# Kernel optimization log

Measured on AMD Instinct MI355X. Metric: run time of the kernel, lower is better.

The kernel has to match this reference:

```python
import jax, jax.numpy as jnp
import numpy as np

ALPHA = 0.2  # LeakyReLU negative slope


def setup_inputs() -> dict:
    key = jax.random.key(0)
    k1, k2, k3, k4 = jax.random.split(key, 4)
    B, N, IN_F, OUT_F = 8, 2048, 128, 64
    inputs = jax.random.normal(k1, (B, N, IN_F), dtype=jnp.float32)
    nodes_embedding = jax.random.normal(k2, (B, N, OUT_F), dtype=jnp.float32)
    # xavier-uniform-like init (gain 1.414)
    limW = 1.414 * np.sqrt(6.0 / (IN_F + OUT_F))
    W = jax.random.uniform(k3, (IN_F, OUT_F), dtype=jnp.float32, minval=-limW, maxval=limW)
    lima = 1.414 * np.sqrt(6.0 / (4 * OUT_F + 1))
    a = jax.random.uniform(k4, (4 * OUT_F, 1), dtype=jnp.float32, minval=-lima, maxval=lima)
    return {"inputs": inputs, "nodes_embedding": nodes_embedding, "W": W, "a": a}


def reference(inputs, nodes_embedding, W, a):
    # x_w: [B,N,F]
    x_w = jnp.matmul(inputs, W)
    # h: [B,N,2F]
    h = jnp.concatenate([nodes_embedding, x_w], axis=2)
    twoF = h.shape[-1]
    # Separable form of concat-based attention: a_input[b,i,j] = [h_i, h_j],
    # so a_input @ a = (h_i . a1) + (h_j . a2). Avoids the O(B*N^2*4F) tensor.
    a1 = a[:twoF, 0]  # [2F]
    a2 = a[twoF:, 0]  # [2F]
    s1 = jnp.einsum('bnf,f->bn', h, a1)  # [B,N]
    s2 = jnp.einsum('bnf,f->bn', h, a2)  # [B,N]
    e = jax.nn.leaky_relu(s1[:, :, None] + s2[:, None, :], negative_slope=ALPHA)  # [B,N,N]
    attention = jax.nn.softmax(e, axis=2)  # softmax over j
    # dropout: eval mode (training=False) -> identity
    h_prime = jnp.matmul(attention, x_w)  # [B,N,F]
    return (jax.nn.relu(h_prime), attention)
```

## Files before the change

### kernel.cpp

```cpp
#include <hip/hip_runtime.h>

#define ALPHA 0.2f
#define B_    8
#define N_    2048
#define INF_  128
#define OUTF_ 64
#define LOG2E 1.4426950408889634f

typedef __attribute__((ext_vector_type(8))) short short8;
typedef __attribute__((ext_vector_type(4))) float f32x4;

__device__ __forceinline__ unsigned short f2bf(float f) {
    unsigned int x = __float_as_uint(f);
    return (unsigned short)((x + 0x7fffu + ((x >> 16) & 1u)) >> 16);
}

__device__ __forceinline__ unsigned int cvtpk_bf16(float lo, float hi) {
    unsigned int r;
    asm("v_cvt_pk_bf16_f32 %0, %1, %2" : "=v"(r) : "v"(lo), "v"(hi));
    return r;
}

__global__ __launch_bounds__(256) void prep_kernel(
    const float* __restrict__ inp,
    const float* __restrict__ nodes,
    const float* __restrict__ Wm,
    const float* __restrict__ av,
    unsigned short* __restrict__ xwT,
    float* __restrict__ s1_out,
    float* __restrict__ s2_out)
{
    __shared__ float w_lds[INF_ * OUTF_];
    __shared__ float in_lds[16 * INF_];
    __shared__ __align__(16) unsigned short t_lds[64 * 16];
    const int tid  = threadIdx.x;
    const int wave = tid >> 6, lane = tid & 63;
    const int r0   = blockIdx.x * 16;

    {
        const float4* Wv = (const float4*)Wm;
        float4* wd = (float4*)w_lds;
        #pragma unroll
        for (int q = 0; q < 8; q++) wd[tid + q * 256] = Wv[tid + q * 256];
        const float4* Iv = (const float4*)(inp + (size_t)r0 * INF_);
        float4* id4 = (float4*)in_lds;
        id4[tid]       = Iv[tid];
        id4[tid + 256] = Iv[tid + 256];
    }
    __syncthreads();

    float acc[4] = {0.f, 0.f, 0.f, 0.f};
    const float* inw = &in_lds[(wave * 4) * INF_];
    #pragma unroll 4
    for (int k = 0; k < INF_; k++) {
        float wv = w_lds[k * OUTF_ + lane];
        acc[0] += inw[k]            * wv;
        acc[1] += inw[INF_ + k]     * wv;
        acc[2] += inw[2 * INF_ + k] * wv;
        acc[3] += inw[3 * INF_ + k] * wv;
    }

    const float a1n = av[lane];
    const float a1x = av[64 + lane];
    const float a2n = av[128 + lane];
    const float a2x = av[192 + lane];

    #pragma unroll
    for (int rr = 0; rr < 4; rr++) {
        const int row = r0 + wave * 4 + rr;
        float nf = nodes[(size_t)row * OUTF_ + lane];
        float p1 = nf * a1n + acc[rr] * a1x;
        float p2 = nf * a2n + acc[rr] * a2x;
        #pragma unroll
        for (int off = 32; off; off >>= 1) {
            p1 += __shfl_down(p1, off);
            p2 += __shfl_down(p2, off);
        }
        if (lane == 0) { s1_out[row] = p1; s2_out[row] = p2; }
        t_lds[lane * 16 + wave * 4 + rr] = f2bf(acc[rr]);
    }
    __syncthreads();

    {
        const int n  = tid >> 2, c0 = (tid & 3) * 4;
        const int b  = r0 >> 11, rb = r0 & (N_ - 1);
        *(uint2*)(xwT + ((size_t)b * OUTF_ + n) * N_ + rb + c0) =
            *(const uint2*)&t_lds[n * 16 + c0];
    }
}

__global__ __launch_bounds__(1024, 4) void attn_kernel(
    const unsigned short* __restrict__ xwT,
    const float* __restrict__ s1g,
    const float* __restrict__ s2g,
    float* __restrict__ out_h,
    float* __restrict__ out_att)
{
    __shared__ __align__(16) float smem[12288];
    __shared__ float s1_lds[64];
    __shared__ float c1_lds[64];
    __shared__ float c2_lds[64];
    __shared__ float redmax[16];

    float* s2L = smem;
    float* s2A = smem + 2048;
    f32x4* red = (f32x4*)smem;

    const int tid  = threadIdx.x;
    const int wave = tid >> 6, lane = tid & 63;
    const int b  = blockIdx.x & 7;
    const int i0 = (blockIdx.x >> 3) << 6;

    {
        float2 v = *(const float2*)(s2g + b * N_ + tid * 2);
        float lm = fmaxf(v.x, v.y);
        s2L[tid * 2]     = v.x * LOG2E;
        s2L[tid * 2 + 1] = v.y * LOG2E;
        s2A[tid * 2]     = v.x * (ALPHA * LOG2E);
        s2A[tid * 2 + 1] = v.y * (ALPHA * LOG2E);
        #pragma unroll
        for (int off = 32; off; off >>= 1) lm = fmaxf(lm, __shfl_xor(lm, off));
        if (lane == 0) redmax[wave] = lm;
    }
    if (tid < 64) s1_lds[tid] = s1g[b * N_ + i0 + tid];
    __syncthreads();

    float s2max = redmax[0];
    #pragma unroll
    for (int w = 1; w < 16; w++) s2max = fmaxf(s2max, redmax[w]);

    {
        const int row = tid >> 4, jo = tid & 15;
        const float s1v = s1_lds[row];
        const float vm  = s1v + s2max;
        const float mL  = (vm > 0.f ? vm : ALPHA * vm) * LOG2E;
        const float d1  = s1v * LOG2E - mL;
        const float d2  = s1v * (ALPHA * LOG2E) - mL;
        float l = 0.f;
        for (int j = jo * 4; j < N_; j += 64) {
            float4 xl = *(const float4*)&s2L[j];
            float4 xa = *(const float4*)&s2A[j];
            l += __builtin_amdgcn_exp2f(fmaxf(d1 + xl.x, d2 + xa.x));
            l += __builtin_amdgcn_exp2f(fmaxf(d1 + xl.y, d2 + xa.y));
            l += __builtin_amdgcn_exp2f(fmaxf(d1 + xl.z, d2 + xa.z));
            l += __builtin_amdgcn_exp2f(fmaxf(d1 + xl.w, d2 + xa.w));
        }
        l += __shfl_xor(l, 1);
        l += __shfl_xor(l, 2);
        l += __shfl_xor(l, 4);
        l += __shfl_xor(l, 8);
        if (jo == 0) {
            const float lg = __builtin_amdgcn_logf(l);
            c1_lds[row] = d1 - lg;
            c2_lds[row] = d2 - lg;
        }
    }
    __syncthreads();

    const int row16 = lane & 15;
    const int quad  = lane >> 4;
    const int wsub  = wave & 3;
    const int jq    = wave >> 2;
    const int irow  = wsub * 16 + row16;
    const float c1  = c1_lds[irow];
    const float c2  = c2_lds[irow];
    const int jb    = jq * 512;

    const unsigned short* bptr[4];
    #pragma unroll
    for (int g = 0; g < 4; g++)
        bptr[g] = xwT + ((size_t)b * OUTF_ + g * 16 + row16) * N_ + jb + quad * 8;

    float* attp = out_att + ((size_t)(b * N_ + i0 + irow)) * N_ + jb + quad * 8;
    const float* pL = s2L + jb + quad * 8;
    const float* pA = s2A + jb + quad * 8;

    f32x4 acc0 = {0.f,0.f,0.f,0.f}, acc1 = {0.f,0.f,0.f,0.f};
    f32x4 acc2 = {0.f,0.f,0.f,0.f}, acc3 = {0.f,0.f,0.f,0.f};

    uint4 bnext[4];
    #pragma unroll
    for (int g = 0; g < 4; g++) bnext[g] = *(const uint4*)bptr[g];

    for (int jt = 0; jt < 512; jt += 32) {
        uint4 bc0 = bnext[0], bc1 = bnext[1], bc2 = bnext[2], bc3 = bnext[3];
        const int jn = (jt + 32) & 511;
        #pragma unroll
        for (int g = 0; g < 4; g++) bnext[g] = *(const uint4*)(bptr[g] + jn);

        float4 sa = *(const float4*)(pL + jt);
        float4 sb = *(const float4*)(pL + jt + 4);
        float4 ta = *(const float4*)(pA + jt);
        float4 tb = *(const float4*)(pA + jt + 4);
        float av8[8];
        av8[0] = __builtin_amdgcn_exp2f(fmaxf(c1 + sa.x, c2 + ta.x));
        av8[1] = __builtin_amdgcn_exp2f(fmaxf(c1 + sa.y, c2 + ta.y));
        av8[2] = __builtin_amdgcn_exp2f(fmaxf(c1 + sa.z, c2 + ta.z));
        av8[3] = __builtin_amdgcn_exp2f(fmaxf(c1 + sa.w, c2 + ta.w));
        av8[4] = __builtin_amdgcn_exp2f(fmaxf(c1 + sb.x, c2 + tb.x));
        av8[5] = __builtin_amdgcn_exp2f(fmaxf(c1 + sb.y, c2 + tb.y));
        av8[6] = __builtin_amdgcn_exp2f(fmaxf(c1 + sb.z, c2 + tb.z));
        av8[7] = __builtin_amdgcn_exp2f(fmaxf(c1 + sb.w, c2 + tb.w));

        *(float4*)(attp + jt)     = make_float4(av8[0], av8[1], av8[2], av8[3]);
        *(float4*)(attp + jt + 4) = make_float4(av8[4], av8[5], av8[6], av8[7]);

        uint4 pk;
        pk.x = cvtpk_bf16(av8[0], av8[1]);
        pk.y = cvtpk_bf16(av8[2], av8[3]);
        pk.z = cvtpk_bf16(av8[4], av8[5]);
        pk.w = cvtpk_bf16(av8[6], av8[7]);
        short8 a8 = *(short8*)&pk;

        acc0 = __builtin_amdgcn_mfma_f32_16x16x32_bf16(a8, *(short8*)&bc0, acc0, 0, 0, 0);
        acc1 = __builtin_amdgcn_mfma_f32_16x16x32_bf16(a8, *(short8*)&bc1, acc1, 0, 0, 0);
        acc2 = __builtin_amdgcn_mfma_f32_16x16x32_bf16(a8, *(short8*)&bc2, acc2, 0, 0, 0);
        acc3 = __builtin_amdgcn_mfma_f32_16x16x32_bf16(a8, *(short8*)&bc3, acc3, 0, 0, 0);
    }

    __syncthreads();
    if (jq > 0) {
        f32x4* p = red + (((jq - 1) * 4 + wsub) * 64 + lane) * 4;
        p[0] = acc0; p[1] = acc1; p[2] = acc2; p[3] = acc3;
    }
    __syncthreads();
    if (jq == 0) {
        #pragma unroll
        for (int q = 0; q < 3; q++) {
            f32x4* p = red + ((q * 4 + wsub) * 64 + lane) * 4;
            acc0 += p[0]; acc1 += p[1]; acc2 += p[2]; acc3 += p[3];
        }
        const size_t hb = ((size_t)(b * N_) + i0 + wsub * 16) * OUTF_;
        #pragma unroll
        for (int r = 0; r < 4; r++) {
            const size_t ro = hb + (size_t)(quad * 4 + r) * OUTF_ + row16;
            out_h[ro]      = fmaxf(acc0[r], 0.f);
            out_h[ro + 16] = fmaxf(acc1[r], 0.f);
            out_h[ro + 32] = fmaxf(acc2[r], 0.f);
            out_h[ro + 48] = fmaxf(acc3[r], 0.f);
        }
    }
}

extern "C" void kernel_launch(void* const* d_in, const int* in_sizes, int n_in,
                              void* d_out, int out_size, void* d_ws, size_t ws_size,
                              hipStream_t stream) {
    const float* inp   = (const float*)d_in[0];
    const float* nodes = (const float*)d_in[1];
    const float* Wm    = (const float*)d_in[2];
    const float* av    = (const float*)d_in[3];

    float* out_h   = (float*)d_out;
    float* out_att = out_h + (size_t)B_ * N_ * OUTF_;

    unsigned short* xwT = (unsigned short*)d_ws;
    float* s1_ws = (float*)((char*)d_ws + (size_t)B_ * OUTF_ * N_ * sizeof(unsigned short));
    float* s2_ws = s1_ws + (size_t)B_ * N_;

    prep_kernel<<<(B_ * N_) / 16, 256, 0, stream>>>(inp, nodes, Wm, av,
                                                    xwT, s1_ws, s2_ws);
    attn_kernel<<<256, 1024, 0, stream>>>(xwT, s1_ws, s2_ws, out_h, out_att);
}
```

Before: 187.7 us.

## Write attention rows in a coalesced pass and vectorize prep matmul LDS reads

The attention-matrix store moves out of the MFMA loop into a separate pass. In that pass each wave writes whole contiguous rows with lane-strided float4 stores, replacing the old pattern of 16 rows by 4 quads per instruction. This is meant to improve write coalescing on the dominant output stream, at the cost of computing the exp values twice and adding an extra barrier. The prep kernel's small matmul also now reads input rows as float4 from LDS, with a 4-way unrolled k loop.

```diff
diff --git a/kernel.cpp b/kernel.cpp
--- a/kernel.cpp
+++ b/kernel.cpp
@@ -31,7 +31,7 @@
     float* __restrict__ s2_out)
 {
     __shared__ float w_lds[INF_ * OUTF_];
-    __shared__ float in_lds[16 * INF_];
+    __shared__ __align__(16) float in_lds[16 * INF_];
     __shared__ __align__(16) unsigned short t_lds[64 * 16];
     const int tid  = threadIdx.x;
     const int wave = tid >> 6, lane = tid & 63;
@@ -51,13 +51,20 @@
 
     float acc[4] = {0.f, 0.f, 0.f, 0.f};
     const float* inw = &in_lds[(wave * 4) * INF_];
-    #pragma unroll 4
-    for (int k = 0; k < INF_; k++) {
-        float wv = w_lds[k * OUTF_ + lane];
-        acc[0] += inw[k]            * wv;
-        acc[1] += inw[INF_ + k]     * wv;
-        acc[2] += inw[2 * INF_ + k] * wv;
-        acc[3] += inw[3 * INF_ + k] * wv;
+    #pragma unroll 2
+    for (int k = 0; k < INF_; k += 4) {
+        float4 r0v = *(const float4*)&inw[k];
+        float4 r1v = *(const float4*)&inw[INF_ + k];
+        float4 r2v = *(const float4*)&inw[2 * INF_ + k];
+        float4 r3v = *(const float4*)&inw[3 * INF_ + k];
+        float w0 = w_lds[k * OUTF_ + lane];
+        float w1 = w_lds[(k + 1) * OUTF_ + lane];
+        float w2 = w_lds[(k + 2) * OUTF_ + lane];
+        float w3 = w_lds[(k + 3) * OUTF_ + lane];
+        acc[0] += r0v.x * w0 + r0v.y * w1 + r0v.z * w2 + r0v.w * w3;
+        acc[1] += r1v.x * w0 + r1v.y * w1 + r1v.z * w2 + r1v.w * w3;
+        acc[2] += r2v.x * w0 + r2v.y * w1 + r2v.z * w2 + r2v.w * w3;
+        acc[3] += r3v.x * w0 + r3v.y * w1 + r3v.z * w2 + r3v.w * w3;
     }
 
     const float a1n = av[lane];
@@ -166,12 +173,44 @@
     const float c2  = c2_lds[irow];
     const int jb    = jq * 512;
 
+    {
+        const size_t rowbase = (size_t)(b * N_ + i0 + wsub * 16);
+        const int cl = lane * 4;
+        for (int r = 0; r < 16; r++) {
+            const float c1r = c1_lds[wsub * 16 + r];
+            const float c2r = c2_lds[wsub * 16 + r];
+            float* orow = out_att + (rowbase + r) * N_ + jb;
+            {
+                const int col = cl;
+                float4 xl = *(const float4*)&s2L[jb + col];
+                float4 xa = *(const float4*)&s2A[jb + col];
+                float4 o;
+                o.x = __builtin_amdgcn_exp2f(fmaxf(c1r + xl.x, c2r + xa.x));
+                o.y = __builtin_amdgcn_exp2f(fmaxf(c1r + xl.y, c2r + xa.y));
+                o.z = __builtin_amdgcn_exp2f(fmaxf(c1r + xl.z, c2r + xa.z));
+                o.w = __builtin_amdgcn_exp2f(fmaxf(c1r + xl.w, c2r + xa.w));
+                *(float4*)(orow + col) = o;
+            }
+            {
+                const int col = 256 + cl;
+                float4 xl = *(const float4*)&s2L[jb + col];
+                float4 xa = *(const float4*)&s2A[jb + col];
+                float4 o;
+                o.x = __builtin_amdgcn_exp2f(fmaxf(c1r + xl.x, c2r + xa.x));
+                o.y = __builtin_amdgcn_exp2f(fmaxf(c1r + xl.y, c2r + xa.y));
+                o.z = __builtin_amdgcn_exp2f(fmaxf(c1r + xl.z, c2r + xa.z));
+                o.w = __builtin_amdgcn_exp2f(fmaxf(c1r + xl.w, c2r + xa.w));
+                *(float4*)(orow + col) = o;
+            }
+        }
+    }
+    __syncthreads();
+
     const unsigned short* bptr[4];
     #pragma unroll
     for (int g = 0; g < 4; g++)
         bptr[g] = xwT + ((size_t)b * OUTF_ + g * 16 + row16) * N_ + jb + quad * 8;
 
-    float* attp = out_att + ((size_t)(b * N_ + i0 + irow)) * N_ + jb + quad * 8;
     const float* pL = s2L + jb + quad * 8;
     const float* pA = s2A + jb + quad * 8;
 
@@ -202,9 +241,6 @@
         av8[6] = __builtin_amdgcn_exp2f(fmaxf(c1 + sb.z, c2 + tb.z));
         av8[7] = __builtin_amdgcn_exp2f(fmaxf(c1 + sb.w, c2 + tb.w));
 
-        *(float4*)(attp + jt)     = make_float4(av8[0], av8[1], av8[2], av8[3]);
-        *(float4*)(attp + jt + 4) = make_float4(av8[4], av8[5], av8[6], av8[7]);
-
         uint4 pk;
         pk.x = cvtpk_bf16(av8[0], av8[1]);
         pk.y = cvtpk_bf16(av8[2], av8[3]);
```

New measurement: 196.9 us. 1.05x slower.
